# Performance work log

Measured on AMD Instinct MI355X. Metric: run time of the kernel, lower is better.

Reference implementation:

```python
import jax, jax.numpy as jnp
import numpy as np

VOCAB = 40000
U = 128  # num_trans_units


def setup_inputs() -> dict:
    key = jax.random.key(0)
    ks = jax.random.split(key, 10)
    B, S, T, L = 16, 512, 64, 64
    sents = jax.random.randint(ks[0], (B, S), 0, 30000)
    triples = jax.random.randint(ks[1], (B, T, L, 3), 0, VOCAB)
    sent_triples = jax.random.randint(ks[2], (B, S, 1), 0, T)
    scale = 0.05
    emb_table = jax.random.normal(ks[3], (VOCAB, U), jnp.float32)
    W_trans = jax.random.normal(ks[4], (U, U), jnp.float32) * scale
    b_trans = jnp.zeros((U,), jnp.float32)
    W_ht = jax.random.normal(ks[5], (2 * U, U), jnp.float32) * scale
    b_ht = jnp.zeros((U,), jnp.float32)
    W_rel = jax.random.normal(ks[6], (U, U), jnp.float32) * scale
    b_rel = jnp.zeros((U,), jnp.float32)
    return {
        "sents": sents, "triples": triples, "sent_triples": sent_triples,
        "emb_table": emb_table,
        "W_trans": W_trans, "b_trans": b_trans,
        "W_ht": W_ht, "b_ht": b_ht,
        "W_rel": W_rel, "b_rel": b_rel,
    }


def reference(sents, triples, sent_triples, emb_table,
              W_trans, b_trans, W_ht, b_ht, W_rel, b_rel):
    # triples: [B, T, L, 3] int ids -> embed [B, T, L, 3, U]
    emb = emb_table[triples]
    # fc_trans_transform: Linear(U,U) + Tanh on last dim
    te = jnp.tanh(emb @ W_trans + b_trans)            # [B,T,L,3,U]
    head, relation, tail = te[..., 0, :], te[..., 1, :], te[..., 2, :]
    head_tail = jnp.concatenate([head, tail], axis=-1)  # [B,T,L,2U]
    ht_t = jnp.tanh(head_tail @ W_ht + b_ht)             # [B,T,L,U]
    rel_t = relation @ W_rel + b_rel                     # [B,T,L,U]
    e_weight = jnp.sum(rel_t * ht_t, axis=-1)            # [B,T,L]
    alpha = jax.nn.softmax(e_weight, axis=-1)            # over triple_len L
    graph_embed = jnp.sum(alpha[..., None] * head_tail, axis=2)  # [B,T,2U]
    # gather_nd: out[b, s] = graph_embed[b, sent_triples[b, s, 0]]
    idx = sent_triples[..., 0]                           # [B,S]
    out = jnp.take_along_axis(graph_embed, idx[:, :, None], axis=1)  # [B,S,2U]
    return out
```

## Files before the change

### kernel.cpp

```cpp
#include <hip/hip_runtime.h>
#include <cstdint>
#include <cstddef>

typedef short short8 __attribute__((ext_vector_type(8)));
typedef float f32x4 __attribute__((ext_vector_type(4)));

#define BB 16
#define SS 512
#define TT 64
#define LL 64
#define UU 128
#define NV 40000

#define WHT_OFF   0u
#define WREL_OFF  (WHT_OFF + 65536u)
#define TE_OFF    (WREL_OFF + 32768u)

__device__ __forceinline__ unsigned short f2bf(float x) {
  unsigned u = __float_as_uint(x);
  unsigned r = ((u >> 16) & 1u) + 0x7FFFu;
  return (unsigned short)((u + r) >> 16);
}
__device__ __forceinline__ float ftanh(float x) {
  float e = __expf(2.0f * x);
  return 1.0f - __fdividef(2.0f, e + 1.0f);
}
__device__ __forceinline__ unsigned cvtpk(float a, float b) {
  unsigned r;
  asm("v_cvt_pk_bf16_f32 %0, %1, %2" : "=v"(r) : "v"(a), "v"(b));
  return r;
}
template<int CTRL>
__device__ __forceinline__ float dpp_mov(float x) {
  return __int_as_float(__builtin_amdgcn_update_dpp(
      0, __float_as_int(x), CTRL, 0xF, 0xF, true));
}
__device__ __forceinline__ float row16_sum(float x) {
  x += dpp_mov<0xB1>(x);
  x += dpp_mov<0x4E>(x);
  x += dpp_mov<0x141>(x);
  x += dpp_mov<0x140>(x);
  return x;
}
__device__ __forceinline__ float full64_sum(float x) {
  x = row16_sum(x);
  x += __shfl_xor(x, 16, 64);
  x += __shfl_xor(x, 32, 64);
  return x;
}
__device__ __forceinline__ float full64_max(float x) {
  x = fmaxf(x, dpp_mov<0xB1>(x));
  x = fmaxf(x, dpp_mov<0x4E>(x));
  x = fmaxf(x, dpp_mov<0x141>(x));
  x = fmaxf(x, dpp_mov<0x140>(x));
  x = fmaxf(x, __shfl_xor(x, 16, 64));
  x = fmaxf(x, __shfl_xor(x, 32, 64));
  return x;
}

__launch_bounds__(512, 8)
__global__ void prep_te(const float* __restrict__ emb_f32,
                        const float* __restrict__ Wt,
                        const float* __restrict__ Wht,
                        const float* __restrict__ Wrel,
                        const float* __restrict__ b_trans,
                        unsigned char* __restrict__ ws,
                        unsigned short* __restrict__ te_g) {
  __shared__ unsigned short TEB[96 * 128];
  const int tid  = threadIdx.x;
  const int base = blockIdx.x * 96;
  const int w    = tid >> 6;
  const int lane = tid & 63;
  const int li   = lane & 15;
  const int lg   = lane >> 4;
  const int nt   = w;

  float4 xv[3], yv[3];
  #pragma unroll
  for (int j = 0; j < 3; ++j) {
    int o = tid + j * 512, row = o >> 4, pc = o & 15;
    int grow = base + row; if (grow > NV - 1) grow = NV - 1;
    int clog = pc ^ (row & 15);
    const float* fb = emb_f32 + (size_t)grow * UU + clog * 8;
    xv[j] = *reinterpret_cast<const float4*>(fb);
    yv[j] = *reinterpret_cast<const float4*>(fb + 4);
  }
  short8 B1h[4];
  #pragma unroll
  for (int kt = 0; kt < 4; ++kt) {
    #pragma unroll
    for (int j = 0; j < 8; ++j)
      B1h[kt][j] = (short)f2bf(Wt[(size_t)(kt * 32 + lg * 8 + j) * UU + nt * 16 + li]);
  }
  #pragma unroll
  for (int j = 0; j < 3; ++j) {
    int o = tid + j * 512;
    uint4 pk = { cvtpk(xv[j].x, xv[j].y), cvtpk(xv[j].z, xv[j].w),
                 cvtpk(yv[j].x, yv[j].y), cvtpk(yv[j].z, yv[j].w) };
    *reinterpret_cast<uint4*>(&TEB[o * 8]) = pk;
  }
  const float4 btr4 = *reinterpret_cast<const float4*>(b_trans + nt * 16 + lg * 4);
  __syncthreads();

  f32x4 acc[6];
  #pragma unroll
  for (int q = 0; q < 6; ++q) acc[q] = f32x4{0.f, 0.f, 0.f, 0.f};
  #pragma unroll
  for (int kt = 0; kt < 4; ++kt) {
    #pragma unroll
    for (int q = 0; q < 6; ++q) {
      const short8 b = *reinterpret_cast<const short8*>(
          &TEB[(q * 16 + li) * 128 + (((kt * 4 + lg) ^ li) << 3)]);
      acc[q] = __builtin_amdgcn_mfma_f32_16x16x32_bf16(B1h[kt], b, acc[q], 0, 0, 0);
    }
  }

  #pragma unroll
  for (int q = 0; q < 6; ++q) {
    int row  = q * 16 + li;
    int grow = base + row; if (grow > NV - 1) grow = NV - 1;
    float v0 = ftanh(acc[q][0] + btr4.x);
    float v1 = ftanh(acc[q][1] + btr4.y);
    float v2 = ftanh(acc[q][2] + btr4.z);
    float v3 = ftanh(acc[q][3] + btr4.w);
    uint2 pk = { cvtpk(v0, v1), cvtpk(v2, v3) };
    *reinterpret_cast<uint2*>(te_g + (size_t)grow * UU + nt * 16 + lg * 4) = pk;
  }

  if (blockIdx.x < 12) {
    int slot = blockIdx.x * 512 + tid;
    const float* W;
    unsigned char* fb;
    if (slot < 4096) { W = Wht;  fb = ws + WHT_OFF; }
    else             { W = Wrel; fb = ws + WREL_OFF; slot -= 4096; }
    int ln = slot & 63, pair = slot >> 6;
    int n  = (pair & 7) * 16 + (ln & 15);
    int k0 = (pair >> 3) * 32 + (ln >> 4) * 8;
    short8 hv;
    #pragma unroll
    for (int j = 0; j < 8; ++j)
      hv[j] = (short)f2bf(W[(size_t)(k0 + j) * UU + n]);
    *reinterpret_cast<short8*>(fb + (size_t)pair * 1024 + ln * 16) = hv;
  }
}

__launch_bounds__(1024, 8)
__global__ void fused_bt(const int* __restrict__ triples,
                         const unsigned short* __restrict__ te_g,
                         const float* __restrict__ b_ht,
                         const float* __restrict__ b_rel,
                         const int* __restrict__ sent_triples,
                         const unsigned char* __restrict__ wsr,
                         float* __restrict__ out) {
  __shared__ unsigned short TEB[192 * 128];
  __shared__ float EWt[8][64];
  __shared__ float PART[8][256];
  __shared__ int MATCH[512];
  __shared__ int NM;

  const int tid  = threadIdx.x;
  const int bt   = blockIdx.x;
  const int w    = tid >> 6;
  const int lane = tid & 63;
  const int li   = lane & 15;
  const int lg   = lane >> 4;
  const int nt   = w & 7;
  const int rh   = w >> 3;

  int tok[3];
  #pragma unroll
  for (int j = 0; j < 3; ++j) {
    int row = (tid + j * 1024) >> 4;
    tok[j] = triples[(size_t)bt * 192 + row];
  }
  int sidx = -1;
  if (tid < SS) sidx = sent_triples[(size_t)(bt >> 6) * SS + tid];
  if (tid == 0) NM = 0;

  short8 sv[3];
  #pragma unroll
  for (int j = 0; j < 3; ++j) {
    int o = tid + j * 1024, row = o >> 4, pc = o & 15;
    int clog = pc ^ (row & 15);
    sv[j] = *reinterpret_cast<const short8*>(
        te_g + (size_t)tok[j] * UU + clog * 8);
  }
  #pragma unroll
  for (int j = 0; j < 3; ++j)
    *reinterpret_cast<short8*>(&TEB[(tid + j * 1024) * 8]) = sv[j];

  const unsigned char* whtb = wsr + WHT_OFF;
  const unsigned char* wrlb = wsr + WREL_OFF;
  const float bhv  = b_ht[nt * 16 + li];
  const float brlv = b_rel[nt * 16 + li];
  short8 Wc = *reinterpret_cast<const short8*>(
      whtb + (size_t)nt * 1024 + lane * 16);
  __syncthreads();

  if (sidx == (bt & 63))
    MATCH[atomicAdd(&NM, 1)] = tid;

  const int mh = rh * 2;
  f32x4 accH[2] = {{0.f,0.f,0.f,0.f},{0.f,0.f,0.f,0.f}};
  f32x4 accR[2] = {{0.f,0.f,0.f,0.f},{0.f,0.f,0.f,0.f}};

  #pragma unroll
  for (int kt = 0; kt < 8; ++kt) {
    short8 Wn;
    if (kt < 7)
      Wn = *reinterpret_cast<const short8*>(
          whtb + (size_t)((kt + 1) * 8 + nt) * 1024 + lane * 16);
    else
      Wn = *reinterpret_cast<const short8*>(
          wrlb + (size_t)nt * 1024 + lane * 16);
    const int koff = (kt < 4) ? 0 : 2;
    const int c16  = (kt & 3) * 4 + lg;
    #pragma unroll
    for (int mi = 0; mi < 2; ++mi) {
      const int row = 48 * (mh + mi) + 3 * li + koff;
      const short8 a = *reinterpret_cast<const short8*>(
          &TEB[row * 128 + ((c16 ^ (row & 15)) << 3)]);
      accH[mi] = __builtin_amdgcn_mfma_f32_16x16x32_bf16(a, Wc, accH[mi], 0, 0, 0);
    }
    Wc = Wn;
  }
  #pragma unroll
  for (int kt = 0; kt < 4; ++kt) {
    short8 Wn;
    if (kt < 3)
      Wn = *reinterpret_cast<const short8*>(
          wrlb + (size_t)((kt + 1) * 8 + nt) * 1024 + lane * 16);
    const int c16 = kt * 4 + lg;
    #pragma unroll
    for (int mi = 0; mi < 2; ++mi) {
      const int row = 48 * (mh + mi) + 3 * li + 1;
      const short8 a = *reinterpret_cast<const short8*>(
          &TEB[row * 128 + ((c16 ^ (row & 15)) << 3)]);
      accR[mi] = __builtin_amdgcn_mfma_f32_16x16x32_bf16(a, Wc, accR[mi], 0, 0, 0);
    }
    Wc = Wn;
  }

  #pragma unroll
  for (int mi = 0; mi < 2; ++mi) {
    #pragma unroll
    for (int r = 0; r < 4; ++r) {
      float p = ftanh(accH[mi][r] + bhv) * (accR[mi][r] + brlv);
      p = row16_sum(p);
      if (li == 0) EWt[nt][(mh + mi) * 16 + lg * 4 + r] = p;
    }
  }
  __syncthreads();

  float alpha;
  {
    float e = 0.f;
    #pragma unroll
    for (int n = 0; n < 8; ++n) e += EWt[n][lane];
    float mx = full64_max(e);
    float ex = __expf(e - mx);
    float sm = full64_sum(ex);
    alpha = ex / sm;
  }

  {
    int cp  = tid & 127, lgp = w >> 1;
    int c0  = cp << 1;
    int k   = (c0 >> 7) << 1;
    int cc  = c0 & 127;
    int w8  = cc >> 3, bofs = (cc & 7) << 1;
    float o0 = 0.f, o1 = 0.f;
    #pragma unroll
    for (int j = 0; j < 8; ++j) {
      int l = lgp * 8 + j;
      float al = __int_as_float(
          __builtin_amdgcn_readlane(__float_as_int(alpha), l));
      int row = 3 * l + k;
      unsigned u = *reinterpret_cast<const unsigned*>(
          reinterpret_cast<const char*>(TEB) + row * 256 +
          (((w8 ^ (row & 15)) << 4) | bofs));
      o0 = fmaf(al, __uint_as_float(u << 16), o0);
      o1 = fmaf(al, __uint_as_float(u & 0xFFFF0000u), o1);
    }
    *reinterpret_cast<float2*>(&PART[lgp][c0]) = make_float2(o0, o1);
  }
  __syncthreads();

  {
    const int b  = bt >> 6;
    const int nm = NM;
    if (w < nm) {
      float4 v = {0.f, 0.f, 0.f, 0.f};
      #pragma unroll
      for (int g = 0; g < 8; ++g) {
        float4 p = reinterpret_cast<const float4*>(&PART[g][0])[lane];
        v.x += p.x; v.y += p.y; v.z += p.z; v.w += p.w;
      }
      for (int q = w; q < nm; q += 16) {
        int s = MATCH[q];
        reinterpret_cast<float4*>(out + ((size_t)(b * SS + s)) * 256)[lane] = v;
      }
    }
  }
}

extern "C" void kernel_launch(void* const* d_in, const int* in_sizes, int n_in,
                              void* d_out, int out_size, void* d_ws, size_t ws_size,
                              hipStream_t stream) {
  const int*   triples      = (const int*)d_in[1];
  const int*   sent_triples = (const int*)d_in[2];
  const float* emb_table    = (const float*)d_in[3];
  const float* W_trans      = (const float*)d_in[4];
  const float* b_trans      = (const float*)d_in[5];
  const float* W_ht         = (const float*)d_in[6];
  const float* b_ht         = (const float*)d_in[7];
  const float* W_rel        = (const float*)d_in[8];
  const float* b_rel        = (const float*)d_in[9];
  float* out = (float*)d_out;
  unsigned char* ws = (unsigned char*)d_ws;
  unsigned short* te_g = (unsigned short*)(ws + TE_OFF);

  prep_te<<<(NV + 95) / 96, 512, 0, stream>>>(
      emb_table, W_trans, W_ht, W_rel, b_trans, ws, te_g);
  fused_bt<<<BB * TT, 1024, 0, stream>>>(
      triples, te_g, b_ht, b_rel, sent_triples, ws, out);
}
```

Before: 40.48 us.

## Process two (b,t) groups per block and prefetch second group's gathers during first GEMM

Each 1024-thread block now handles two consecutive (b,t) triple groups instead of one, halving the grid to 512 blocks. The gather of the second group's te rows is issued into registers right after the first group's MFMA pass, and stored to LDS after the first softmax, so its latency overlaps compute. It also shares the sent_triples scan across both groups. The cost is fewer blocks for latency hiding, more registers, and extra barriers per block.

```diff
diff --git a/kernel.cpp b/kernel.cpp
--- a/kernel.cpp
+++ b/kernel.cpp
@@ -144,6 +144,110 @@
   }
 }
 
+__device__ __forceinline__ void gemm2_ew(
+    const unsigned short* TEB, const unsigned char* whtb,
+    const unsigned char* wrlb, short8 Wc, int nt, int mh, int li, int lg,
+    int lane, float bhv, float brlv, float (*EWt)[64]) {
+  f32x4 accH[2] = {{0.f,0.f,0.f,0.f},{0.f,0.f,0.f,0.f}};
+  f32x4 accR[2] = {{0.f,0.f,0.f,0.f},{0.f,0.f,0.f,0.f}};
+  #pragma unroll
+  for (int kt = 0; kt < 8; ++kt) {
+    short8 Wn;
+    if (kt < 7)
+      Wn = *reinterpret_cast<const short8*>(
+          whtb + (size_t)((kt + 1) * 8 + nt) * 1024 + lane * 16);
+    else
+      Wn = *reinterpret_cast<const short8*>(
+          wrlb + (size_t)nt * 1024 + lane * 16);
+    const int koff = (kt < 4) ? 0 : 2;
+    const int c16  = (kt & 3) * 4 + lg;
+    #pragma unroll
+    for (int mi = 0; mi < 2; ++mi) {
+      const int row = 48 * (mh + mi) + 3 * li + koff;
+      const short8 a = *reinterpret_cast<const short8*>(
+          &TEB[row * 128 + ((c16 ^ (row & 15)) << 3)]);
+      accH[mi] = __builtin_amdgcn_mfma_f32_16x16x32_bf16(a, Wc, accH[mi], 0, 0, 0);
+    }
+    Wc = Wn;
+  }
+  #pragma unroll
+  for (int kt = 0; kt < 4; ++kt) {
+    short8 Wn;
+    if (kt < 3)
+      Wn = *reinterpret_cast<const short8*>(
+          wrlb + (size_t)((kt + 1) * 8 + nt) * 1024 + lane * 16);
+    const int c16 = kt * 4 + lg;
+    #pragma unroll
+    for (int mi = 0; mi < 2; ++mi) {
+      const int row = 48 * (mh + mi) + 3 * li + 1;
+      const short8 a = *reinterpret_cast<const short8*>(
+          &TEB[row * 128 + ((c16 ^ (row & 15)) << 3)]);
+      accR[mi] = __builtin_amdgcn_mfma_f32_16x16x32_bf16(a, Wc, accR[mi], 0, 0, 0);
+    }
+    Wc = Wn;
+  }
+  #pragma unroll
+  for (int mi = 0; mi < 2; ++mi) {
+    #pragma unroll
+    for (int r = 0; r < 4; ++r) {
+      float p = ftanh(accH[mi][r] + bhv) * (accR[mi][r] + brlv);
+      p = row16_sum(p);
+      if (li == 0) EWt[nt][(mh + mi) * 16 + lg * 4 + r] = p;
+    }
+  }
+}
+
+__device__ __forceinline__ void softmax_wsum(
+    const float (*EWt)[64], float (*PART)[256], const unsigned short* TEB,
+    int tid, int w, int lane) {
+  float alpha;
+  {
+    float e = 0.f;
+    #pragma unroll
+    for (int n = 0; n < 8; ++n) e += EWt[n][lane];
+    float mx = full64_max(e);
+    float ex = __expf(e - mx);
+    float sm = full64_sum(ex);
+    alpha = ex / sm;
+  }
+  int cp  = tid & 127, lgp = w >> 1;
+  int c0  = cp << 1;
+  int k   = (c0 >> 7) << 1;
+  int cc  = c0 & 127;
+  int w8  = cc >> 3, bofs = (cc & 7) << 1;
+  float o0 = 0.f, o1 = 0.f;
+  #pragma unroll
+  for (int j = 0; j < 8; ++j) {
+    int l = lgp * 8 + j;
+    float al = __int_as_float(
+        __builtin_amdgcn_readlane(__float_as_int(alpha), l));
+    int row = 3 * l + k;
+    unsigned u = *reinterpret_cast<const unsigned*>(
+        reinterpret_cast<const char*>(TEB) + row * 256 +
+        (((w8 ^ (row & 15)) << 4) | bofs));
+    o0 = fmaf(al, __uint_as_float(u << 16), o0);
+    o1 = fmaf(al, __uint_as_float(u & 0xFFFF0000u), o1);
+  }
+  *reinterpret_cast<float2*>(&PART[lgp][c0]) = make_float2(o0, o1);
+}
+
+__device__ __forceinline__ void scatter_out(
+    const float (*PART)[256], const int* match, int nm, int b, int w,
+    int lane, float* out) {
+  if (w < nm) {
+    float4 v = {0.f, 0.f, 0.f, 0.f};
+    #pragma unroll
+    for (int g = 0; g < 8; ++g) {
+      float4 p = reinterpret_cast<const float4*>(&PART[g][0])[lane];
+      v.x += p.x; v.y += p.y; v.z += p.z; v.w += p.w;
+    }
+    for (int q = w; q < nm; q += 16) {
+      int s = match[q];
+      reinterpret_cast<float4*>(out + ((size_t)(b * SS + s)) * 256)[lane] = v;
+    }
+  }
+}
+
 __launch_bounds__(1024, 8)
 __global__ void fused_bt(const int* __restrict__ triples,
                          const unsigned short* __restrict__ te_g,
@@ -155,39 +259,45 @@
   __shared__ unsigned short TEB[192 * 128];
   __shared__ float EWt[8][64];
   __shared__ float PART[8][256];
-  __shared__ int MATCH[512];
-  __shared__ int NM;
+  __shared__ int MATCH[2][512];
+  __shared__ int NM[2];
 
   const int tid  = threadIdx.x;
-  const int bt   = blockIdx.x;
+  const int bt0  = blockIdx.x * 2;
   const int w    = tid >> 6;
   const int lane = tid & 63;
   const int li   = lane & 15;
   const int lg   = lane >> 4;
   const int nt   = w & 7;
   const int rh   = w >> 3;
-
-  int tok[3];
+  const int mh   = rh * 2;
+  const int b    = bt0 >> 6;
+  const int t0   = bt0 & 63;
+
+  int tok0[3], tok1[3];
   #pragma unroll
   for (int j = 0; j < 3; ++j) {
     int row = (tid + j * 1024) >> 4;
-    tok[j] = triples[(size_t)bt * 192 + row];
+    tok0[j] = triples[(size_t)bt0 * 192 + row];
+    tok1[j] = triples[(size_t)(bt0 + 1) * 192 + row];
   }
   int sidx = -1;
-  if (tid < SS) sidx = sent_triples[(size_t)(bt >> 6) * SS + tid];
-  if (tid == 0) NM = 0;
-
-  short8 sv[3];
-  #pragma unroll
-  for (int j = 0; j < 3; ++j) {
-    int o = tid + j * 1024, row = o >> 4, pc = o & 15;
-    int clog = pc ^ (row & 15);
-    sv[j] = *reinterpret_cast<const short8*>(
-        te_g + (size_t)tok[j] * UU + clog * 8);
-  }
-  #pragma unroll
-  for (int j = 0; j < 3; ++j)
-    *reinterpret_cast<short8*>(&TEB[(tid + j * 1024) * 8]) = sv[j];
+  if (tid < SS) sidx = sent_triples[(size_t)b * SS + tid];
+  if (tid < 2) NM[tid] = 0;
+
+  {
+    short8 sv[3];
+    #pragma unroll
+    for (int j = 0; j < 3; ++j) {
+      int o = tid + j * 1024, row = o >> 4, pc = o & 15;
+      int clog = pc ^ (row & 15);
+      sv[j] = *reinterpret_cast<const short8*>(
+          te_g + (size_t)tok0[j] * UU + clog * 8);
+    }
+    #pragma unroll
+    for (int j = 0; j < 3; ++j)
+      *reinterpret_cast<short8*>(&TEB[(tid + j * 1024) * 8]) = sv[j];
+  }
 
   const unsigned char* whtb = wsr + WHT_OFF;
   const unsigned char* wrlb = wsr + WREL_OFF;
@@ -197,111 +307,39 @@
       whtb + (size_t)nt * 1024 + lane * 16);
   __syncthreads();
 
-  if (sidx == (bt & 63))
-    MATCH[atomicAdd(&NM, 1)] = tid;
-
-  const int mh = rh * 2;
-  f32x4 accH[2] = {{0.f,0.f,0.f,0.f},{0.f,0.f,0.f,0.f}};
-  f32x4 accR[2] = {{0.f,0.f,0.f,0.f},{0.f,0.f,0.f,0.f}};
-
-  #pragma unroll
-  for (int kt = 0; kt < 8; ++kt) {
-    short8 Wn;
-    if (kt < 7)
-      Wn = *reinterpret_cast<const short8*>(
-          whtb + (size_t)((kt + 1) * 8 + nt) * 1024 + lane * 16);
-    else
-      Wn = *reinterpret_cast<const short8*>(
-          wrlb + (size_t)nt * 1024 + lane * 16);
-    const int koff = (kt < 4) ? 0 : 2;
-    const int c16  = (kt & 3) * 4 + lg;
-    #pragma unroll
-    for (int mi = 0; mi < 2; ++mi) {
-      const int row = 48 * (mh + mi) + 3 * li + koff;
-      const short8 a = *reinterpret_cast<const short8*>(
-          &TEB[row * 128 + ((c16 ^ (row & 15)) << 3)]);
-      accH[mi] = __builtin_amdgcn_mfma_f32_16x16x32_bf16(a, Wc, accH[mi], 0, 0, 0);
-    }
-    Wc = Wn;
-  }
-  #pragma unroll
-  for (int kt = 0; kt < 4; ++kt) {
-    short8 Wn;
-    if (kt < 3)
-      Wn = *reinterpret_cast<const short8*>(
-          wrlb + (size_t)((kt + 1) * 8 + nt) * 1024 + lane * 16);
-    const int c16 = kt * 4 + lg;
-    #pragma unroll
-    for (int mi = 0; mi < 2; ++mi) {
-      const int row = 48 * (mh + mi) + 3 * li + 1;
-      const short8 a = *reinterpret_cast<const short8*>(
-          &TEB[row * 128 + ((c16 ^ (row & 15)) << 3)]);
-      accR[mi] = __builtin_amdgcn_mfma_f32_16x16x32_bf16(a, Wc, accR[mi], 0, 0, 0);
-    }
-    Wc = Wn;
-  }
-
-  #pragma unroll
-  for (int mi = 0; mi < 2; ++mi) {
-    #pragma unroll
-    for (int r = 0; r < 4; ++r) {
-      float p = ftanh(accH[mi][r] + bhv) * (accR[mi][r] + brlv);
-      p = row16_sum(p);
-      if (li == 0) EWt[nt][(mh + mi) * 16 + lg * 4 + r] = p;
-    }
-  }
-  __syncthreads();
-
-  float alpha;
-  {
-    float e = 0.f;
-    #pragma unroll
-    for (int n = 0; n < 8; ++n) e += EWt[n][lane];
-    float mx = full64_max(e);
-    float ex = __expf(e - mx);
-    float sm = full64_sum(ex);
-    alpha = ex / sm;
-  }
-
-  {
-    int cp  = tid & 127, lgp = w >> 1;
-    int c0  = cp << 1;
-    int k   = (c0 >> 7) << 1;
-    int cc  = c0 & 127;
-    int w8  = cc >> 3, bofs = (cc & 7) << 1;
-    float o0 = 0.f, o1 = 0.f;
-    #pragma unroll
-    for (int j = 0; j < 8; ++j) {
-      int l = lgp * 8 + j;
-      float al = __int_as_float(
-          __builtin_amdgcn_readlane(__float_as_int(alpha), l));
-      int row = 3 * l + k;
-      unsigned u = *reinterpret_cast<const unsigned*>(
-          reinterpret_cast<const char*>(TEB) + row * 256 +
-          (((w8 ^ (row & 15)) << 4) | bofs));
-      o0 = fmaf(al, __uint_as_float(u << 16), o0);
-      o1 = fmaf(al, __uint_as_float(u & 0xFFFF0000u), o1);
-    }
-    *reinterpret_cast<float2*>(&PART[lgp][c0]) = make_float2(o0, o1);
-  }
-  __syncthreads();
-
-  {
-    const int b  = bt >> 6;
-    const int nm = NM;
-    if (w < nm) {
-      float4 v = {0.f, 0.f, 0.f, 0.f};
-      #pragma unroll
-      for (int g = 0; g < 8; ++g) {
-        float4 p = reinterpret_cast<const float4*>(&PART[g][0])[lane];
-        v.x += p.x; v.y += p.y; v.z += p.z; v.w += p.w;
-      }
-      for (int q = w; q < nm; q += 16) {
-        int s = MATCH[q];
-        reinterpret_cast<float4*>(out + ((size_t)(b * SS + s)) * 256)[lane] = v;
-      }
-    }
-  }
+  if (sidx == t0)     MATCH[0][atomicAdd(&NM[0], 1)] = tid;
+  if (sidx == t0 + 1) MATCH[1][atomicAdd(&NM[1], 1)] = tid;
+
+  gemm2_ew(TEB, whtb, wrlb, Wc, nt, mh, li, lg, lane, bhv, brlv, EWt);
+
+  short8 sv1[3];
+  #pragma unroll
+  for (int j = 0; j < 3; ++j) {
+    int o = tid + j * 1024, row = o >> 4, pc = o & 15;
+    int clog = pc ^ (row & 15);
+    sv1[j] = *reinterpret_cast<const short8*>(
+        te_g + (size_t)tok1[j] * UU + clog * 8);
+  }
+  __syncthreads();
+
+  softmax_wsum(EWt, PART, TEB, tid, w, lane);
+  __syncthreads();
+
+  #pragma unroll
+  for (int j = 0; j < 3; ++j)
+    *reinterpret_cast<short8*>(&TEB[(tid + j * 1024) * 8]) = sv1[j];
+  Wc = *reinterpret_cast<const short8*>(
+      whtb + (size_t)nt * 1024 + lane * 16);
+  scatter_out(PART, MATCH[0], NM[0], b, w, lane, out);
+  __syncthreads();
+
+  gemm2_ew(TEB, whtb, wrlb, Wc, nt, mh, li, lg, lane, bhv, brlv, EWt);
+  __syncthreads();
+
+  softmax_wsum(EWt, PART, TEB, tid, w, lane);
+  __syncthreads();
+
+  scatter_out(PART, MATCH[1], NM[1], b, w, lane, out);
 }
 
 extern "C" void kernel_launch(void* const* d_in, const int* in_sizes, int n_in,
@@ -322,6 +360,6 @@
 
   prep_te<<<(NV + 95) / 96, 512, 0, stream>>>(
       emb_table, W_trans, W_ht, W_rel, b_trans, ws, te_g);
-  fused_bt<<<BB * TT, 1024, 0, stream>>>(
+  fused_bt<<<BB * TT / 2, 1024, 0, stream>>>(
       triples, te_g, b_ht, b_rel, sent_triples, ws, out);
 }
```

Result: slower. 51.64 us (+27.6%).
